# Optimization experiments

Measured on AMD Instinct MI355X. Metric: run time of the kernel, lower is better.

Reference implementation:

```python
import jax, jax.numpy as jnp
import numpy as np

N = 100000        # nodes in the batched graph
E = 1_600_000     # directed edges
G = 256           # graphs in the batch
IN, H = 3, 64
EPS = 1e-5        # BatchNorm eps (eval mode: running stats, dropout off)


def setup_inputs() -> dict:
    key = jax.random.key(0)
    ks = jax.random.split(key, 40)
    inp = {}
    inp["x"] = jax.random.normal(ks[0], (N, IN), jnp.float32)
    inp["edge_index"] = jax.random.randint(ks[1], (2, E), 0, N, dtype=jnp.int32)
    inp["batch_idx"] = jnp.sort(jax.random.randint(ks[2], (N,), 0, G, dtype=jnp.int32))
    dims = [IN, H, H, H]  # zip(dims[:-1], dims[1:]) -> 3 GCN layers (as in source)
    k = 3
    for i in range(3):
        inp[f"W{i}"] = jax.random.normal(ks[k], (dims[i], dims[i + 1]), jnp.float32) * 0.1; k += 1
        inp[f"b{i}"] = jax.random.normal(ks[k], (dims[i + 1],), jnp.float32) * 0.01; k += 1
        inp[f"g{i}"] = jax.random.uniform(ks[k], (dims[i + 1],), jnp.float32, 0.5, 1.5); k += 1
        inp[f"be{i}"] = jax.random.normal(ks[k], (dims[i + 1],), jnp.float32) * 0.1; k += 1
        inp[f"rm{i}"] = jax.random.normal(ks[k], (dims[i + 1],), jnp.float32) * 0.1; k += 1
        inp[f"rv{i}"] = jax.random.uniform(ks[k], (dims[i + 1],), jnp.float32, 0.5, 1.5); k += 1
    inp["mW1"] = jax.random.normal(ks[k], (2 * H, 32), jnp.float32) * 0.1; k += 1
    inp["mb1"] = jnp.zeros((32,), jnp.float32)
    inp["mW2"] = jax.random.normal(ks[k], (32, 16), jnp.float32) * 0.1; k += 1
    inp["mb2"] = jnp.zeros((16,), jnp.float32)
    inp["mW3"] = jax.random.normal(ks[k], (16, 1), jnp.float32) * 0.1; k += 1
    inp["mb3"] = jnp.zeros((1,), jnp.float32)
    return inp


def _gcn(x, W, b, src, dst):
    # PyG GCNConv: add self-loops, symmetric D^-1/2 (A+I) D^-1/2 normalization
    h = x @ W                                   # [N, out]
    deg = jnp.zeros((N,), h.dtype).at[dst].add(1.0) + 1.0  # +1 self-loop
    dinv = jax.lax.rsqrt(deg)
    coef = dinv[src] * dinv[dst]                # [E]
    agg = jax.ops.segment_sum(h[src] * coef[:, None], dst, num_segments=N)
    agg = agg + h * (dinv * dinv)[:, None]      # self-loop message
    return agg + b


def _bn(x, g, be, rm, rv):
    return (x - rm) * jax.lax.rsqrt(rv + EPS) * g + be


def _forward(x, edge_index, batch_idx,
             W0, b0, g0, be0, rm0, rv0,
             W1, b1, g1, be1, rm1, rv1,
             W2, b2, g2, be2, rm2, rv2,
             mW1, mb1, mW2, mb2, mW3, mb3):
    src, dst = edge_index[0], edge_index[1]
    layers = [(W0, b0, g0, be0, rm0, rv0), (W1, b1, g1, be1, rm1, rv1), (W2, b2, g2, be2, rm2, rv2)]
    for (W, b, g, be, rm, rv) in layers:
        x = jax.nn.relu(_bn(_gcn(x, W, b, src, dst), g, be, rm, rv))
    cnt = jax.ops.segment_sum(jnp.ones((N,), x.dtype), batch_idx, num_segments=G)
    x_mean = jax.ops.segment_sum(x, batch_idx, num_segments=G) / jnp.maximum(cnt, 1.0)[:, None]
    x_max = jax.ops.segment_max(x, batch_idx, num_segments=G)
    x_max = jnp.where(jnp.isfinite(x_max), x_max, 0.0)
    xg = jnp.concatenate([x_mean, x_max], axis=1)  # [G, 2H]
    h = jax.nn.relu(xg @ mW1 + mb1)
    h = jax.nn.relu(h @ mW2 + mb2)
    return h @ mW3 + mb3                            # [G, 1]


def reference(x, edge_index, batch_idx,
              W0, b0, g0, be0, rm0, rv0,
              W1, b1, g1, be1, rm1, rv1,
              W2, b2, g2, be2, rm2, rv2,
              mW1, mb1, mW2, mb2, mW3, mb3):
    return _forward(x, edge_index, batch_idx,
                    W0, b0, g0, be0, rm0, rv0,
                    W1, b1, g1, be1, rm1, rv1,
                    W2, b2, g2, be2, rm2, rv2,
                    mW1, mb1, mW2, mb2, mW3, mb3)
```

## Files before the change

### kernel.cpp

```cpp
#include <hip/hip_runtime.h>
#include <hip/hip_fp16.h>

#define NN 100000
#define EE 1600000
#define GG 256
#define EPS 1e-5f
#define KB2 ((NN + 511) >> 9)
#define BCAP 10240
#define EPB 4096
#define EBLK ((EE + EPB - 1) / EPB)
#define NB256 ((NN + 255) / 256)

__device__ __forceinline__ unsigned int pack2(float x, float y) {
  __half2 h = __float22half2_rn(make_float2(x, y));
  return *reinterpret_cast<unsigned int*>(&h);
}
__device__ __forceinline__ uint2 pack4(float x, float y, float z, float w) {
  uint2 r;
  r.x = pack2(x, y);
  r.y = pack2(z, w);
  return r;
}
__device__ __forceinline__ void add8(float4& a0, float4& a1, uint4 v) {
  __half2 h0 = *reinterpret_cast<__half2*>(&v.x);
  __half2 h1 = *reinterpret_cast<__half2*>(&v.y);
  __half2 h2 = *reinterpret_cast<__half2*>(&v.z);
  __half2 h3 = *reinterpret_cast<__half2*>(&v.w);
  float2 f0 = __half22float2(h0), f1 = __half22float2(h1);
  float2 f2 = __half22float2(h2), f3 = __half22float2(h3);
  a0.x += f0.x; a0.y += f0.y; a0.z += f1.x; a0.w += f1.y;
  a1.x += f2.x; a1.y += f2.y; a1.z += f3.x; a1.w += f3.y;
}

__device__ __forceinline__ void gld16(uint4& d, const uint4* p) {
  asm volatile("global_load_dwordx4 %0, %1, off" : "=v"(d) : "v"(p));
}
__device__ __forceinline__ void gldf16(float4& d, const float4* p) {
  asm volatile("global_load_dwordx4 %0, %1, off" : "=v"(d) : "v"(p));
}

__global__ void k_passA(const int* __restrict__ ei, int* __restrict__ bfill,
                        int* __restrict__ tmp) {
  __shared__ int cnt[KB2], cur[KB2], base[KB2];
  int t = threadIdx.x;
  for (int b = t; b < KB2; b += 256) { cnt[b] = 0; cur[b] = 0; }
  __syncthreads();
  int e0 = blockIdx.x * EPB;
  int myb[16], myp[16];
#pragma unroll
  for (int j = 0; j < 16; ++j) {
    int e = e0 + j * 256 + t;
    int bb = -1, pp = 0;
    if (e < EE) {
      int ss = ei[e];
      int dd = ei[EE + e];
      bb = dd >> 9;
      pp = (ss << 9) | (dd & 511);
    }
    myb[j] = bb;
    myp[j] = pp;
    if (bb >= 0) atomicAdd(&cnt[bb], 1);
  }
  __syncthreads();
  for (int b = t; b < KB2; b += 256)
    if (cnt[b] > 0) base[b] = b * BCAP + atomicAdd(&bfill[b], cnt[b]);
  __syncthreads();
#pragma unroll
  for (int j = 0; j < 16; ++j) {
    int bb = myb[j];
    if (bb >= 0) {
      int slot = base[bb] + atomicAdd(&cur[bb], 1);
      tmp[slot] = myp[j];
    }
  }
}

__global__ void k_bucket(const int* __restrict__ tmp, const int* __restrict__ bfill,
                         const float* __restrict__ x, int* __restrict__ csr,
                         int* __restrict__ row, int* __restrict__ rowe,
                         float* __restrict__ dinv, float4* __restrict__ xd) {
  __shared__ int cnt[512], s[512], fillp[512];
  __shared__ int stmp[BCAP];
  int b = blockIdx.x, t = threadIdx.x;
  int nb = b << 9;
  int e0 = b * BCAP;
  int fill = bfill[b];
  cnt[t] = 0;
  cnt[t + 256] = 0;
  for (int e = t; e < fill; e += 256) stmp[e] = tmp[e0 + e];
  __syncthreads();
  for (int e = t; e < fill; e += 256) atomicAdd(&cnt[stmp[e] & 511], 1);
  __syncthreads();
  s[t] = cnt[t];
  s[t + 256] = cnt[t + 256];
  __syncthreads();
  for (int off = 1; off < 512; off <<= 1) {
    int i1 = t + 256;
    int v0 = (t >= off) ? s[t - off] : 0;
    int v1 = (i1 >= off) ? s[i1 - off] : 0;
    __syncthreads();
    s[t] += v0;
    s[i1] += v1;
    __syncthreads();
  }
#pragma unroll
  for (int k = 0; k < 2; ++k) {
    int i = t + k * 256;
    int excl = s[i] - cnt[i];
    fillp[i] = excl;
    int dst = nb + i;
    if (dst < NN) {
      row[dst] = e0 + excl;
      rowe[dst] = e0 + s[i];
      float d = rsqrtf((float)cnt[i] + 1.0f);
      dinv[dst] = d;
      xd[dst] = make_float4(x[dst * 3] * d, x[dst * 3 + 1] * d, x[dst * 3 + 2] * d, 0.f);
    }
  }
  __syncthreads();
  for (int e = t; e < fill; e += 256) {
    int ed = stmp[e];
    int slot = atomicAdd(&fillp[ed & 511], 1);
    csr[e0 + slot] = ed >> 9;
  }
}

__launch_bounds__(256, 4)
__global__ void k_agg3f(const float4* __restrict__ xd, const int* __restrict__ row,
                        const int* __restrict__ rowe, const int* __restrict__ csr,
                        const float* __restrict__ dinv,
                        const float* __restrict__ W, const float* __restrict__ b,
                        const float* __restrict__ gam, const float* __restrict__ bet,
                        const float* __restrict__ rm, const float* __restrict__ rv,
                        uint2* __restrict__ out) {
  int n = blockIdx.x * 256 + threadIdx.x;
  if (n >= NN) return;
  int s0 = row[n], s1 = rowe[n];
  float4 a = xd[n];
  float ax = a.x, ay = a.y, az = a.z;
  for (int i = s0; i < s1; i += 16) {
    int idx[16];
#pragma unroll
    for (int j = 0; j < 16; ++j) idx[j] = csr[min(i + j, s1 - 1)];
    float4 v[16];
#pragma unroll
    for (int j = 0; j < 16; ++j) gldf16(v[j], xd + idx[j]);
    asm volatile("s_waitcnt vmcnt(0)" ::: "memory");
    __builtin_amdgcn_sched_barrier(0);
    int rem = s1 - i;
#pragma unroll
    for (int j = 0; j < 16; ++j)
      if (j < rem) { ax += v[j].x; ay += v[j].y; az += v[j].z; }
  }
  float d = dinv[n];
  float t0 = ax * d, t1 = ay * d, t2 = az * d;
  const float4* W4 = (const float4*)W;
  const float4* b4 = (const float4*)b;
  const float4* g4p = (const float4*)gam;
  const float4* be4p = (const float4*)bet;
  const float4* rm4p = (const float4*)rm;
  const float4* rv4p = (const float4*)rv;
#pragma unroll
  for (int c4 = 0; c4 < 16; ++c4) {
    float4 w0 = W4[c4], w1 = W4[16 + c4], w2 = W4[32 + c4];
    float4 bb = b4[c4], g4 = g4p[c4], be4 = be4p[c4], rm4 = rm4p[c4], rv4 = rv4p[c4];
    float4 o;
    o.x = fmaf(t0, w0.x, fmaf(t1, w1.x, fmaf(t2, w2.x, bb.x)));
    o.y = fmaf(t0, w0.y, fmaf(t1, w1.y, fmaf(t2, w2.y, bb.y)));
    o.z = fmaf(t0, w0.z, fmaf(t1, w1.z, fmaf(t2, w2.z, bb.z)));
    o.w = fmaf(t0, w0.w, fmaf(t1, w1.w, fmaf(t2, w2.w, bb.w)));
    float scx = g4.x * rsqrtf(rv4.x + EPS), shx = be4.x - rm4.x * scx;
    float scy = g4.y * rsqrtf(rv4.y + EPS), shy = be4.y - rm4.y * scy;
    float scz = g4.z * rsqrtf(rv4.z + EPS), shz = be4.z - rm4.z * scz;
    float scw = g4.w * rsqrtf(rv4.w + EPS), shw = be4.w - rm4.w * scw;
    o.x = fmaxf(fmaf(o.x, scx, shx), 0.f) * d;
    o.y = fmaxf(fmaf(o.y, scy, shy), 0.f) * d;
    o.z = fmaxf(fmaf(o.z, scz, shz), 0.f) * d;
    o.w = fmaxf(fmaf(o.w, scw, shw), 0.f) * d;
    out[(size_t)n * 16 + c4] = pack4(o.x, o.y, o.z, o.w);
  }
}

template <bool MID>
__launch_bounds__(256, 4)
__global__ void k_layer2(const uint4* __restrict__ xs, const int* __restrict__ row,
                         const int* __restrict__ rowe, const int* __restrict__ csr,
                         const float* __restrict__ dinv,
                         const float* __restrict__ W, const float* __restrict__ b,
                         const float* __restrict__ gam, const float* __restrict__ bet,
                         const float* __restrict__ rm, const float* __restrict__ rv,
                         uint4* __restrict__ outv, const int* __restrict__ bidx,
                         float* __restrict__ xsum, unsigned* __restrict__ xmaxu) {
  __shared__ float sh[32][68];
  int t = blockIdx.x * 256 + threadIdx.x;
  int n = t >> 3, sub = t & 7;
  int local = threadIdx.x >> 3;
  int s0 = row[n], s1 = rowe[n];
  float4 a0 = make_float4(0.f, 0.f, 0.f, 0.f);
  float4 a1 = make_float4(0.f, 0.f, 0.f, 0.f);
  add8(a0, a1, xs[(size_t)n * 8 + sub]);
  if (s0 < s1) {
    int e = s0 + sub;
    int myidx = (e < s1) ? csr[e] : n;
    for (int i = s0; i < s1; i += 8) {
      int e2 = i + 8 + sub;
      int pre = csr[min(e2, s1 - 1)];
      uint4 v0, v1, v2, v3, v4, v5, v6, v7;
      gld16(v0, xs + ((size_t)__shfl(myidx, 0, 8) * 8 + sub));
      gld16(v1, xs + ((size_t)__shfl(myidx, 1, 8) * 8 + sub));
      gld16(v2, xs + ((size_t)__shfl(myidx, 2, 8) * 8 + sub));
      gld16(v3, xs + ((size_t)__shfl(myidx, 3, 8) * 8 + sub));
      gld16(v4, xs + ((size_t)__shfl(myidx, 4, 8) * 8 + sub));
      gld16(v5, xs + ((size_t)__shfl(myidx, 5, 8) * 8 + sub));
      gld16(v6, xs + ((size_t)__shfl(myidx, 6, 8) * 8 + sub));
      gld16(v7, xs + ((size_t)__shfl(myidx, 7, 8) * 8 + sub));
      asm volatile("s_waitcnt vmcnt(0)" ::: "memory");
      __builtin_amdgcn_sched_barrier(0);
      int rem = s1 - i;
      add8(a0, a1, v0);
      if (rem > 1) add8(a0, a1, v1);
      if (rem > 2) add8(a0, a1, v2);
      if (rem > 3) add8(a0, a1, v3);
      if (rem > 4) add8(a0, a1, v4);
      if (rem > 5) add8(a0, a1, v5);
      if (rem > 6) add8(a0, a1, v6);
      if (rem > 7) add8(a0, a1, v7);
      myidx = (e2 < s1) ? pre : n;
    }
  }
  float d = dinv[n];
  float4 w0 = make_float4(a0.x * d, a0.y * d, a0.z * d, a0.w * d);
  float4 w1 = make_float4(a1.x * d, a1.y * d, a1.z * d, a1.w * d);
  *(float4*)&sh[local][sub * 8] = w0;
  *(float4*)&sh[local][sub * 8 + 4] = w1;
  __syncthreads();
  const float4* W4 = (const float4*)W;
  float4 accA = ((const float4*)b)[sub * 2];
  float4 accB = ((const float4*)b)[sub * 2 + 1];
#pragma unroll 8
  for (int k = 0; k < 64; ++k) {
    float xv = sh[local][k];
    float4 wA = W4[k * 16 + sub * 2];
    float4 wB = W4[k * 16 + sub * 2 + 1];
    accA.x = fmaf(xv, wA.x, accA.x);
    accA.y = fmaf(xv, wA.y, accA.y);
    accA.z = fmaf(xv, wA.z, accA.z);
    accA.w = fmaf(xv, wA.w, accA.w);
    accB.x = fmaf(xv, wB.x, accB.x);
    accB.y = fmaf(xv, wB.y, accB.y);
    accB.z = fmaf(xv, wB.z, accB.z);
    accB.w = fmaf(xv, wB.w, accB.w);
  }
  float4 gA = ((const float4*)gam)[sub * 2], gB = ((const float4*)gam)[sub * 2 + 1];
  float4 beA = ((const float4*)bet)[sub * 2], beB = ((const float4*)bet)[sub * 2 + 1];
  float4 rmA = ((const float4*)rm)[sub * 2], rmB = ((const float4*)rm)[sub * 2 + 1];
  float4 rvA = ((const float4*)rv)[sub * 2], rvB = ((const float4*)rv)[sub * 2 + 1];
  float4 oA, oB;
  {
    float sc = gA.x * rsqrtf(rvA.x + EPS); oA.x = fmaxf(fmaf(accA.x, sc, beA.x - rmA.x * sc), 0.f);
    sc = gA.y * rsqrtf(rvA.y + EPS); oA.y = fmaxf(fmaf(accA.y, sc, beA.y - rmA.y * sc), 0.f);
    sc = gA.z * rsqrtf(rvA.z + EPS); oA.z = fmaxf(fmaf(accA.z, sc, beA.z - rmA.z * sc), 0.f);
    sc = gA.w * rsqrtf(rvA.w + EPS); oA.w = fmaxf(fmaf(accA.w, sc, beA.w - rmA.w * sc), 0.f);
    sc = gB.x * rsqrtf(rvB.x + EPS); oB.x = fmaxf(fmaf(accB.x, sc, beB.x - rmB.x * sc), 0.f);
    sc = gB.y * rsqrtf(rvB.y + EPS); oB.y = fmaxf(fmaf(accB.y, sc, beB.y - rmB.y * sc), 0.f);
    sc = gB.z * rsqrtf(rvB.z + EPS); oB.z = fmaxf(fmaf(accB.z, sc, beB.z - rmB.z * sc), 0.f);
    sc = gB.w * rsqrtf(rvB.w + EPS); oB.w = fmaxf(fmaf(accB.w, sc, beB.w - rmB.w * sc), 0.f);
  }
  if (MID) {
    uint4 r;
    r.x = pack2(oA.x * d, oA.y * d);
    r.y = pack2(oA.z * d, oA.w * d);
    r.z = pack2(oB.x * d, oB.y * d);
    r.w = pack2(oB.z * d, oB.w * d);
    outv[(size_t)n * 8 + sub] = r;
  } else {
    __syncthreads();
    *(float4*)&sh[local][sub * 8] = oA;
    *(float4*)&sh[local][sub * 8 + 4] = oB;
    __syncthreads();
    int c = threadIdx.x & 63, q = threadIdx.x >> 6;
    int nb = blockIdx.x * 32 + q * 8;
    float ps = 0.f, pm = 0.f;
    int curg = bidx[nb];
#pragma unroll
    for (int r2 = 0; r2 < 8; ++r2) {
      int g = bidx[nb + r2];
      if (g != curg) {
        atomicAdd(&xsum[(size_t)curg * 64 + c], ps);
        atomicMax(&xmaxu[(size_t)curg * 64 + c], __float_as_uint(pm));
        ps = 0.f; pm = 0.f; curg = g;
      }
      float v = sh[q * 8 + r2][c];
      ps += v;
      pm = fmaxf(pm, v);
    }
    atomicAdd(&xsum[(size_t)curg * 64 + c], ps);
    atomicMax(&xmaxu[(size_t)curg * 64 + c], __float_as_uint(pm));
  }
}

__device__ __forceinline__ int lower_bound(const int* __restrict__ b, int target) {
  int lo = 0, hi = NN;
  while (lo < hi) {
    int m = (lo + hi) >> 1;
    if (b[m] < target) lo = m + 1; else hi = m;
  }
  return lo;
}

__global__ void k_mlp(const float* __restrict__ xsum, const float* __restrict__ xmaxf,
                      const int* __restrict__ bidx,
                      const float* __restrict__ mW1, const float* __restrict__ mb1,
                      const float* __restrict__ mW2, const float* __restrict__ mb2,
                      const float* __restrict__ mW3, const float* __restrict__ mb3,
                      float* __restrict__ out) {
  __shared__ float xg[128], h1[32], h2[16];
  int g = blockIdx.x, t = threadIdx.x;
  int lo = lower_bound(bidx, g);
  int hi = lower_bound(bidx, g + 1);
  float inv = 1.0f / fmaxf((float)(hi - lo), 1.0f);
  xg[t] = xsum[(size_t)g * 64 + t] * inv;
  xg[64 + t] = xmaxf[(size_t)g * 64 + t];
  __syncthreads();
  if (t < 32) {
    float a = mb1[t];
    for (int k = 0; k < 128; ++k) a = fmaf(xg[k], mW1[k * 32 + t], a);
    h1[t] = fmaxf(a, 0.f);
  }
  __syncthreads();
  if (t < 16) {
    float a = mb2[t];
    for (int k = 0; k < 32; ++k) a = fmaf(h1[k], mW2[k * 16 + t], a);
    h2[t] = fmaxf(a, 0.f);
  }
  __syncthreads();
  if (t == 0) {
    float a = mb3[0];
    for (int k = 0; k < 16; ++k) a = fmaf(h2[k], mW3[k], a);
    out[g] = a;
  }
}

extern "C" void kernel_launch(void* const* d_in, const int* in_sizes, int n_in,
                              void* d_out, int out_size, void* d_ws, size_t ws_size,
                              hipStream_t stream) {
  const float* x = (const float*)d_in[0];
  const int* ei = (const int*)d_in[1];
  const int* bidx = (const int*)d_in[2];
  const float *W[3], *b[3], *gam[3], *bet[3], *rm[3], *rv[3];
  for (int l = 0; l < 3; ++l) {
    W[l] = (const float*)d_in[3 + 6 * l];
    b[l] = (const float*)d_in[4 + 6 * l];
    gam[l] = (const float*)d_in[5 + 6 * l];
    bet[l] = (const float*)d_in[6 + 6 * l];
    rm[l] = (const float*)d_in[7 + 6 * l];
    rv[l] = (const float*)d_in[8 + 6 * l];
  }
  const float* mW1 = (const float*)d_in[21];
  const float* mb1 = (const float*)d_in[22];
  const float* mW2 = (const float*)d_in[23];
  const float* mb2 = (const float*)d_in[24];
  const float* mW3 = (const float*)d_in[25];
  const float* mb3 = (const float*)d_in[26];
  float* out = (float*)d_out;

  char* ws = (char*)d_ws;
  size_t off = 0;
  auto alloc = [&](size_t bytes) {
    void* p = ws + off;
    off = (off + bytes + 1023) & ~(size_t)1023;
    return p;
  };
  float* dinv = (float*)alloc(NN * 4);
  int* row = (int*)alloc(NN * 4);
  int* rowe = (int*)alloc(NN * 4);
  int* csr = (int*)alloc((size_t)KB2 * BCAP * 4);
  int* bfill = (int*)alloc(256 * 4);
  float4* xd = (float4*)alloc((size_t)NN * 16);
  float* pool = (float*)alloc(GG * 64 * 4 * 2);
  float* xsum = pool;
  unsigned* xmaxu = (unsigned*)(pool + GG * 64);
  float* bufA = (float*)alloc((size_t)NN * 64 * 4);
  float* bufB = (float*)alloc((size_t)NN * 64 * 2);
  int* tmp = (int*)bufA;

  hipMemsetAsync(bfill, 0, 256 * 4, stream);
  hipMemsetAsync(pool, 0, GG * 64 * 4 * 2, stream);

  k_passA<<<EBLK, 256, 0, stream>>>(ei, bfill, tmp);
  k_bucket<<<KB2, 256, 0, stream>>>(tmp, bfill, x, csr, row, rowe, dinv, xd);

  int nb8 = (NN * 8) / 256;

  k_agg3f<<<NB256, 256, 0, stream>>>(xd, row, rowe, csr, dinv, W[0], b[0], gam[0], bet[0],
                                     rm[0], rv[0], (uint2*)bufA);
  k_layer2<true><<<nb8, 256, 0, stream>>>((const uint4*)bufA, row, rowe, csr, dinv, W[1], b[1],
                                          gam[1], bet[1], rm[1], rv[1], (uint4*)bufB,
                                          bidx, xsum, xmaxu);
  k_layer2<false><<<nb8, 256, 0, stream>>>((const uint4*)bufB, row, rowe, csr, dinv, W[2], b[2],
                                           gam[2], bet[2], rm[2], rv[2], (uint4*)bufA,
                                           bidx, xsum, xmaxu);
  k_mlp<<<GG, 64, 0, stream>>>(xsum, (const float*)xmaxu, bidx, mW1, mb1, mW2, mb2,
                               mW3, mb3, out);
}
```

Baseline: 318.6 us.

## Split layer-1 aggregation across four lanes per node and widen bucket blocks

```diff
diff --git a/kernel.cpp b/kernel.cpp
--- a/kernel.cpp
+++ b/kernel.cpp
@@ -86,39 +86,31 @@
   int e0 = b * BCAP;
   int fill = bfill[b];
   cnt[t] = 0;
-  cnt[t + 256] = 0;
-  for (int e = t; e < fill; e += 256) stmp[e] = tmp[e0 + e];
-  __syncthreads();
-  for (int e = t; e < fill; e += 256) atomicAdd(&cnt[stmp[e] & 511], 1);
-  __syncthreads();
-  s[t] = cnt[t];
-  s[t + 256] = cnt[t + 256];
+  for (int e = t; e < fill; e += 512) stmp[e] = tmp[e0 + e];
+  __syncthreads();
+  for (int e = t; e < fill; e += 512) atomicAdd(&cnt[stmp[e] & 511], 1);
+  __syncthreads();
+  int c = cnt[t];
+  s[t] = c;
   __syncthreads();
   for (int off = 1; off < 512; off <<= 1) {
-    int i1 = t + 256;
-    int v0 = (t >= off) ? s[t - off] : 0;
-    int v1 = (i1 >= off) ? s[i1 - off] : 0;
+    int v = (t >= off) ? s[t - off] : 0;
     __syncthreads();
-    s[t] += v0;
-    s[i1] += v1;
+    s[t] += v;
     __syncthreads();
   }
-#pragma unroll
-  for (int k = 0; k < 2; ++k) {
-    int i = t + k * 256;
-    int excl = s[i] - cnt[i];
-    fillp[i] = excl;
-    int dst = nb + i;
-    if (dst < NN) {
-      row[dst] = e0 + excl;
-      rowe[dst] = e0 + s[i];
-      float d = rsqrtf((float)cnt[i] + 1.0f);
-      dinv[dst] = d;
-      xd[dst] = make_float4(x[dst * 3] * d, x[dst * 3 + 1] * d, x[dst * 3 + 2] * d, 0.f);
-    }
-  }
-  __syncthreads();
-  for (int e = t; e < fill; e += 256) {
+  int excl = s[t] - c;
+  fillp[t] = excl;
+  int dst = nb + t;
+  if (dst < NN) {
+    row[dst] = e0 + excl;
+    rowe[dst] = e0 + s[t];
+    float d = rsqrtf((float)c + 1.0f);
+    dinv[dst] = d;
+    xd[dst] = make_float4(x[dst * 3] * d, x[dst * 3 + 1] * d, x[dst * 3 + 2] * d, 0.f);
+  }
+  __syncthreads();
+  for (int e = t; e < fill; e += 512) {
     int ed = stmp[e];
     int slot = atomicAdd(&fillp[ed & 511], 1);
     csr[e0 + slot] = ed >> 9;
@@ -133,25 +125,30 @@
                         const float* __restrict__ gam, const float* __restrict__ bet,
                         const float* __restrict__ rm, const float* __restrict__ rv,
                         uint2* __restrict__ out) {
-  int n = blockIdx.x * 256 + threadIdx.x;
+  int t = blockIdx.x * 256 + threadIdx.x;
+  int n = t >> 2, q = t & 3;
   if (n >= NN) return;
   int s0 = row[n], s1 = rowe[n];
   float4 a = xd[n];
-  float ax = a.x, ay = a.y, az = a.z;
+  float ax, ay, az;
+  if (q == 0) { ax = a.x; ay = a.y; az = a.z; } else { ax = 0.f; ay = 0.f; az = 0.f; }
   for (int i = s0; i < s1; i += 16) {
-    int idx[16];
-#pragma unroll
-    for (int j = 0; j < 16; ++j) idx[j] = csr[min(i + j, s1 - 1)];
-    float4 v[16];
-#pragma unroll
-    for (int j = 0; j < 16; ++j) gldf16(v[j], xd + idx[j]);
+    int base = i + q * 4;
+    int idx[4];
+#pragma unroll
+    for (int j = 0; j < 4; ++j) idx[j] = csr[min(base + j, s1 - 1)];
+    float4 v[4];
+#pragma unroll
+    for (int j = 0; j < 4; ++j) gldf16(v[j], xd + idx[j]);
     asm volatile("s_waitcnt vmcnt(0)" ::: "memory");
     __builtin_amdgcn_sched_barrier(0);
-    int rem = s1 - i;
-#pragma unroll
-    for (int j = 0; j < 16; ++j)
-      if (j < rem) { ax += v[j].x; ay += v[j].y; az += v[j].z; }
-  }
+#pragma unroll
+    for (int j = 0; j < 4; ++j)
+      if (base + j < s1) { ax += v[j].x; ay += v[j].y; az += v[j].z; }
+  }
+  ax += __shfl_xor(ax, 1); ax += __shfl_xor(ax, 2);
+  ay += __shfl_xor(ay, 1); ay += __shfl_xor(ay, 2);
+  az += __shfl_xor(az, 1); az += __shfl_xor(az, 2);
   float d = dinv[n];
   float t0 = ax * d, t1 = ay * d, t2 = az * d;
   const float4* W4 = (const float4*)W;
@@ -161,7 +158,8 @@
   const float4* rm4p = (const float4*)rm;
   const float4* rv4p = (const float4*)rv;
 #pragma unroll
-  for (int c4 = 0; c4 < 16; ++c4) {
+  for (int k = 0; k < 4; ++k) {
+    int c4 = q * 4 + k;
     float4 w0 = W4[c4], w1 = W4[16 + c4], w2 = W4[32 + c4];
     float4 bb = b4[c4], g4 = g4p[c4], be4 = be4p[c4], rm4 = rm4p[c4], rv4 = rv4p[c4];
     float4 o;
@@ -388,12 +386,13 @@
   hipMemsetAsync(pool, 0, GG * 64 * 4 * 2, stream);
 
   k_passA<<<EBLK, 256, 0, stream>>>(ei, bfill, tmp);
-  k_bucket<<<KB2, 256, 0, stream>>>(tmp, bfill, x, csr, row, rowe, dinv, xd);
+  k_bucket<<<KB2, 512, 0, stream>>>(tmp, bfill, x, csr, row, rowe, dinv, xd);
 
   int nb8 = (NN * 8) / 256;
-
-  k_agg3f<<<NB256, 256, 0, stream>>>(xd, row, rowe, csr, dinv, W[0], b[0], gam[0], bet[0],
-                                     rm[0], rv[0], (uint2*)bufA);
+  int nb4 = (NN * 4 + 255) / 256;
+
+  k_agg3f<<<nb4, 256, 0, stream>>>(xd, row, rowe, csr, dinv, W[0], b[0], gam[0], bet[0],
+                                   rm[0], rv[0], (uint2*)bufA);
   k_layer2<true><<<nb8, 256, 0, stream>>>((const uint4*)bufA, row, rowe, csr, dinv, W[1], b[1],
                                           gam[1], bet[1], rm[1], rv[1], (uint4*)bufB,
                                           bidx, xsum, xmaxu);
```

Result: no change. 320.6 us (+0.6%).

## Double-buffer neighbor gathers in layer-2 aggregation with software pipelining

Applied to the files above, without the earlier changes.

```diff
diff --git a/kernel.cpp b/kernel.cpp
--- a/kernel.cpp
+++ b/kernel.cpp
@@ -37,6 +37,9 @@
 }
 __device__ __forceinline__ void gldf16(float4& d, const float4* p) {
   asm volatile("global_load_dwordx4 %0, %1, off" : "=v"(d) : "v"(p));
+}
+__device__ __forceinline__ void gld4(int& d, const int* p) {
+  asm volatile("global_load_dword %0, %1, off" : "=v"(d) : "v"(p));
 }
 
 __global__ void k_passA(const int* __restrict__ ei, int* __restrict__ bfill,
@@ -181,6 +184,30 @@
   }
 }
 
+#define ISSUE_BATCH(CREG_DST, CREG_SRC, V0, V1, V2, V3, V4, V5, V6, V7, IBASE)          \
+  gld4(CREG_DST, csr + min((IBASE) + 16 + sub, s1 - 1));                                 \
+  gld16(V0, xs + ((size_t)__shfl(CREG_SRC, 0, 8) * 8 + sub));                            \
+  gld16(V1, xs + ((size_t)__shfl(CREG_SRC, 1, 8) * 8 + sub));                            \
+  gld16(V2, xs + ((size_t)__shfl(CREG_SRC, 2, 8) * 8 + sub));                            \
+  gld16(V3, xs + ((size_t)__shfl(CREG_SRC, 3, 8) * 8 + sub));                            \
+  gld16(V4, xs + ((size_t)__shfl(CREG_SRC, 4, 8) * 8 + sub));                            \
+  gld16(V5, xs + ((size_t)__shfl(CREG_SRC, 5, 8) * 8 + sub));                            \
+  gld16(V6, xs + ((size_t)__shfl(CREG_SRC, 6, 8) * 8 + sub));                            \
+  gld16(V7, xs + ((size_t)__shfl(CREG_SRC, 7, 8) * 8 + sub));
+
+#define CONSUME8(V0, V1, V2, V3, V4, V5, V6, V7)                                         \
+  {                                                                                      \
+    int rem = s1 - i;                                                                    \
+    add8(a0, a1, V0);                                                                    \
+    if (rem > 1) add8(a0, a1, V1);                                                       \
+    if (rem > 2) add8(a0, a1, V2);                                                       \
+    if (rem > 3) add8(a0, a1, V3);                                                       \
+    if (rem > 4) add8(a0, a1, V4);                                                       \
+    if (rem > 5) add8(a0, a1, V5);                                                       \
+    if (rem > 6) add8(a0, a1, V6);                                                       \
+    if (rem > 7) add8(a0, a1, V7);                                                       \
+  }
+
 template <bool MID>
 __launch_bounds__(256, 4)
 __global__ void k_layer2(const uint4* __restrict__ xs, const int* __restrict__ row,
@@ -198,36 +225,37 @@
   int s0 = row[n], s1 = rowe[n];
   float4 a0 = make_float4(0.f, 0.f, 0.f, 0.f);
   float4 a1 = make_float4(0.f, 0.f, 0.f, 0.f);
+  if (s0 < s1) {
+    int c0, cA, cB;
+    gld4(c0, csr + min(s0 + sub, s1 - 1));
+    asm volatile("s_waitcnt vmcnt(0)" ::: "memory");
+    __builtin_amdgcn_sched_barrier(0);
+    uint4 vA0, vA1, vA2, vA3, vA4, vA5, vA6, vA7;
+    uint4 vB0, vB1, vB2, vB3, vB4, vB5, vB6, vB7;
+    ISSUE_BATCH(cA, c0, vA0, vA1, vA2, vA3, vA4, vA5, vA6, vA7, s0 - 8);
+    int i = s0;
+    while (true) {
+      asm volatile("s_waitcnt vmcnt(8)" ::: "memory");
+      __builtin_amdgcn_sched_barrier(0);
+      ISSUE_BATCH(cB, cA, vB0, vB1, vB2, vB3, vB4, vB5, vB6, vB7, i);
+      asm volatile("s_waitcnt vmcnt(9)" ::: "memory");
+      __builtin_amdgcn_sched_barrier(0);
+      CONSUME8(vA0, vA1, vA2, vA3, vA4, vA5, vA6, vA7);
+      i += 8;
+      if (i >= s1) break;
+      asm volatile("s_waitcnt vmcnt(8)" ::: "memory");
+      __builtin_amdgcn_sched_barrier(0);
+      ISSUE_BATCH(cA, cB, vA0, vA1, vA2, vA3, vA4, vA5, vA6, vA7, i);
+      asm volatile("s_waitcnt vmcnt(9)" ::: "memory");
+      __builtin_amdgcn_sched_barrier(0);
+      CONSUME8(vB0, vB1, vB2, vB3, vB4, vB5, vB6, vB7);
+      i += 8;
+      if (i >= s1) break;
+    }
+    asm volatile("s_waitcnt vmcnt(0)" ::: "memory");
+    __builtin_amdgcn_sched_barrier(0);
+  }
   add8(a0, a1, xs[(size_t)n * 8 + sub]);
-  if (s0 < s1) {
-    int e = s0 + sub;
-    int myidx = (e < s1) ? csr[e] : n;
-    for (int i = s0; i < s1; i += 8) {
-      int e2 = i + 8 + sub;
-      int pre = csr[min(e2, s1 - 1)];
-      uint4 v0, v1, v2, v3, v4, v5, v6, v7;
-      gld16(v0, xs + ((size_t)__shfl(myidx, 0, 8) * 8 + sub));
-      gld16(v1, xs + ((size_t)__shfl(myidx, 1, 8) * 8 + sub));
-      gld16(v2, xs + ((size_t)__shfl(myidx, 2, 8) * 8 + sub));
-      gld16(v3, xs + ((size_t)__shfl(myidx, 3, 8) * 8 + sub));
-      gld16(v4, xs + ((size_t)__shfl(myidx, 4, 8) * 8 + sub));
-      gld16(v5, xs + ((size_t)__shfl(myidx, 5, 8) * 8 + sub));
-      gld16(v6, xs + ((size_t)__shfl(myidx, 6, 8) * 8 + sub));
-      gld16(v7, xs + ((size_t)__shfl(myidx, 7, 8) * 8 + sub));
-      asm volatile("s_waitcnt vmcnt(0)" ::: "memory");
-      __builtin_amdgcn_sched_barrier(0);
-      int rem = s1 - i;
-      add8(a0, a1, v0);
-      if (rem > 1) add8(a0, a1, v1);
-      if (rem > 2) add8(a0, a1, v2);
-      if (rem > 3) add8(a0, a1, v3);
-      if (rem > 4) add8(a0, a1, v4);
-      if (rem > 5) add8(a0, a1, v5);
-      if (rem > 6) add8(a0, a1, v6);
-      if (rem > 7) add8(a0, a1, v7);
-      myidx = (e2 < s1) ? pre : n;
-    }
-  }
   float d = dinv[n];
   float4 w0 = make_float4(a0.x * d, a0.y * d, a0.z * d, a0.w * d);
   float4 w1 = make_float4(a1.x * d, a1.y * d, a1.z * d, a1.w * d);
```

New measurement: 323.7 us. No clear change (+1.6%).
